# Kernel optimization log

Measured on AMD Instinct MI355X. Metric: run time of the kernel, lower is better.

## Reference

```python
import jax, jax.numpy as jnp
import numpy as np

NUM_HEADS = 16
NUM_BUCKETS = 32
MAX_DISTANCE = 128


def _rel_bucket(rel):
    # bidirectional T5-style relative position bucketing
    nb = NUM_BUCKETS // 2
    ret = (rel > 0).astype(jnp.int32) * nb
    n = jnp.abs(rel)
    max_exact = nb // 2
    is_small = n < max_exact
    safe = jnp.maximum(n, 1).astype(jnp.float32)
    large = max_exact + (jnp.log(safe / max_exact) / np.log(MAX_DISTANCE / max_exact) * (nb - max_exact)).astype(jnp.int32)
    large = jnp.minimum(large, nb - 1)
    return ret + jnp.where(is_small, n, large)


def setup_inputs() -> dict:
    key = jax.random.key(0)
    ks = jax.random.split(key, 12)
    S, B, E = 1024, 4, 1024
    D = E // NUM_HEADS
    s = 0.02
    return {
        "query": jax.random.normal(ks[0], (S, B, E), jnp.float32),
        "q_w": jax.random.normal(ks[1], (E, E), jnp.float32) * s,
        "q_b": jnp.zeros((E,), jnp.float32),
        "k_w": jax.random.normal(ks[2], (E, E), jnp.float32) * s,
        "k_b": jnp.zeros((E,), jnp.float32),
        "v_w": jax.random.normal(ks[3], (E, E), jnp.float32) * s,
        "v_b": jnp.zeros((E,), jnp.float32),
        "out_w": jax.random.normal(ks[4], (E, E), jnp.float32) * s,
        "out_b": jnp.zeros((E,), jnp.float32),
        "rel_emb": jax.random.normal(ks[5], (NUM_BUCKETS, NUM_HEADS), jnp.float32) * s,
        "grep_w": jax.random.normal(ks[6], (8, D), jnp.float32) * s,
        "grep_b": jnp.zeros((8,), jnp.float32),
        "grep_a": jnp.ones((NUM_HEADS,), jnp.float32),
    }


def reference(query, q_w, q_b, k_w, k_b, v_w, v_b, out_w, out_b, rel_emb, grep_w, grep_b, grep_a):
    S, B, E = query.shape
    H = NUM_HEADS
    D = E // H
    scaling = D ** -0.5

    q = (query @ q_w.T + q_b) * scaling  # scaling applied before gating, as in WavLM
    k = query @ k_w.T + k_b
    v = query @ v_w.T + v_b

    def split(x):  # (S,B,E) -> (B,H,S,D)
        return x.reshape(S, B, H, D).transpose(1, 2, 0, 3)

    q4, k4, v4 = split(q), split(k), split(v)

    attn = jnp.einsum('bhqd,bhkd->bhqk', q4, k4)  # (B,H,S,S)

    pos = jnp.arange(S)
    bucket = _rel_bucket(pos[None, :] - pos[:, None])  # (S,S)
    pbias = rel_emb[bucket].transpose(2, 0, 1)          # (H,S,S)

    # GRU-gated relative position scaling
    g = jnp.einsum('bhsd,ed->bhse', q4, grep_w) + grep_b      # (B,H,S,8)
    g = jax.nn.sigmoid(g.reshape(B, H, S, 2, 4).sum(-1))     # (B,H,S,2)
    gate_a, gate_b = g[..., 0], g[..., 1]
    gate = gate_a * (gate_b * grep_a[None, :, None] - 1.0) + 2.0  # (B,H,S)

    attn = attn + gate[..., None] * pbias[None]
    probs = jax.nn.softmax(attn, axis=-1)
    ctx = jnp.einsum('bhqk,bhkd->bhqd', probs, v4)  # (B,H,S,D)
    out = ctx.transpose(2, 0, 1, 3).reshape(S, B, E) @ out_w.T + out_b
    return out
```

## Files before the change

### kernel.cpp

```cpp
#include <hip/hip_runtime.h>
#include <hip/hip_bf16.h>
#include <stdint.h>


typedef short bf16x8 __attribute__((ext_vector_type(8)));
typedef _Float16 f16x8 __attribute__((ext_vector_type(8)));
typedef float f32x4 __attribute__((ext_vector_type(4)));
typedef float f32x16 __attribute__((ext_vector_type(16)));
typedef unsigned uint32x2 __attribute__((ext_vector_type(2)));

#define MFMA_BF16(a, b, c) __builtin_amdgcn_mfma_f32_16x16x32_bf16((a), (b), (c), 0, 0, 0)
#define MFMA_F16(a, b, c) __builtin_amdgcn_mfma_f32_16x16x32_f16((a), (b), (c), 0, 0, 0)
#define MFMA32_BF16(a, b, c) __builtin_amdgcn_mfma_f32_32x32x16_bf16((a), (b), (c), 0, 0, 0)

#define LOG2E 1.44269504088896f
#define LN2 0.693147180559945f

__device__ __forceinline__ unsigned short f2bf(float x) {
  union { float f; unsigned u; } v; v.f = x;
  unsigned r = v.u + 0x7fffu + ((v.u >> 16) & 1u);
  return (unsigned short)(r >> 16);
}
__device__ __forceinline__ float bf2f(unsigned short u) {
  union { unsigned u; float f; } v; v.u = ((unsigned)u) << 16;
  return v.f;
}
__device__ __forceinline__ unsigned short f2h(float x) {
  union { _Float16 h; unsigned short u; } v; v.h = (_Float16)x;
  return v.u;
}
__device__ __forceinline__ unsigned pk_bf2(float a, float b) {
  union { __hip_bfloat162 h2; unsigned u; } v;
  v.h2 = __float22bfloat162_rn(float2{a, b});
  return v.u;
}

__device__ __forceinline__ void gload_lds16(const void* g, void* l) {
  __builtin_amdgcn_global_load_lds(
      (const __attribute__((address_space(1))) unsigned int*)g,
      (__attribute__((address_space(3))) unsigned int*)l, 16, 0, 0);
}

__device__ __forceinline__ int swz(int row) { return (row ^ (row >> 2)) & 3; }

__global__ __launch_bounds__(256) void prep_kernel(
    const float* __restrict__ query, const float* __restrict__ q_w,
    const float* __restrict__ k_w, const float* __restrict__ v_w,
    const float* __restrict__ out_w, const float* __restrict__ rel_emb,
    unsigned short* __restrict__ q_bf, unsigned short* __restrict__ wq,
    unsigned short* __restrict__ wk, unsigned short* __restrict__ wv,
    unsigned short* __restrict__ ow_h,
    float* __restrict__ bias_f) {
  int i = blockIdx.x * 256 + threadIdx.x;
  if (i < 1048576) {
    int e4 = (i & 255) << 2;
    int sb = i >> 8;
    int s = sb >> 2, b = sb & 3;
    float4 q4 = *(const float4*)(query + ((size_t)i << 2));
    ushort4 o;
    o.x = f2bf(q4.x); o.y = f2bf(q4.y); o.z = f2bf(q4.z); o.w = f2bf(q4.w);
    *(ushort4*)&q_bf[((size_t)(b * 1024 + s) << 10) | e4] = o;
  } else if (i < 1310720) {
    int j = (i - 1048576) << 2;
    float4 a = *(const float4*)(q_w + j);
    float4 b = *(const float4*)(k_w + j);
    float4 c = *(const float4*)(v_w + j);
    float4 d = *(const float4*)(out_w + j);
    ushort4 o;
    o.x = f2bf(a.x); o.y = f2bf(a.y); o.z = f2bf(a.z); o.w = f2bf(a.w);
    *(ushort4*)&wq[j] = o;
    o.x = f2bf(b.x); o.y = f2bf(b.y); o.z = f2bf(b.z); o.w = f2bf(b.w);
    *(ushort4*)&wk[j] = o;
    o.x = f2bf(c.x); o.y = f2bf(c.y); o.z = f2bf(c.z); o.w = f2bf(c.w);
    *(ushort4*)&wv[j] = o;
    o.x = f2h(d.x); o.y = f2h(d.y); o.z = f2h(d.z); o.w = f2h(d.w);
    *(ushort4*)&ow_h[j] = o;
  } else {
    int idx = i - 1310720;
    if (idx >= 2056) return;
    if (idx >= 2047) {
#pragma unroll
      for (int h = 0; h < 16; ++h) bias_f[h * 2056 + idx] = 0.f;
      return;
    }
    int rel = idx - 1023;
    int n = rel < 0 ? -rel : rel;
    int ret = rel > 0 ? 16 : 0;
    int bucket;
    if (n < 8) {
      bucket = ret + n;
    } else {
      int large = 8 + (int)(logf((float)n / 8.0f) / logf(16.0f) * 8.0f);
      if (large > 15) large = 15;
      bucket = ret + large;
    }
#pragma unroll
    for (int h = 0; h < 16; ++h)
      bias_f[h * 2056 + idx] = rel_emb[bucket * 16 + h] * LOG2E;
  }
}

__global__ __launch_bounds__(256, 3) void qkv_gemm_kernel(
    const unsigned short* __restrict__ A, const unsigned short* __restrict__ Wq,
    const unsigned short* __restrict__ Wk, const unsigned short* __restrict__ Wv,
    const float* __restrict__ qb, const float* __restrict__ kb, const float* __restrict__ vb,
    unsigned short* __restrict__ qh,
    unsigned short* __restrict__ kh,
    unsigned short* __restrict__ vT)
{
  __shared__ __align__(16) char smem[32768];
  const int tid = threadIdx.x, lane = tid & 63;
  const int wv_ = tid >> 6;
  const int nt = blockIdx.x;
  const int mt = blockIdx.y;
  const int mat = nt >> 3;
  const unsigned short* W = mat == 0 ? Wq : (mat == 1 ? Wk : Wv);
  const int n0 = (nt & 7) * 128;
  const int m0 = mt * 128;
  const int moff = (wv_ & 1) * 64;
  const int noff = (wv_ >> 1) * 64;
  const int q15 = lane & 15, quad = lane >> 4;

  const int abase = (mat < 2) ? 8192 : 0;
  const int bbase2 = 8192 - abase;
  const int aoff = (mat < 2) ? noff : moff;
  const int boff = (mat < 2) ? moff : noff;

  f32x4 acc[4][4] = {};
  const char* Ab = (const char*)A;
  const char* Wb = (const char*)W;

  int st_row[2], st_g[2];
#pragma unroll
  for (int c = 0; c < 2; ++c) {
    int o = c * 4096 + tid * 16;
    int row = o >> 6, p = (o >> 4) & 3;
    st_row[c] = row;
    st_g[c] = p ^ swz(row);
  }

#define QKV_STAGE(kt, buf)                                                     \
  {                                                                            \
    char* bb = smem + (buf)*16384;                                             \
    _Pragma("unroll") for (int c = 0; c < 2; ++c) {                            \
      int o = c * 4096 + tid * 16;                                             \
      size_t ga = (size_t)(m0 + st_row[c]) * 2048 + (size_t)(kt)*64 + st_g[c] * 16; \
      size_t gb = (size_t)(n0 + st_row[c]) * 2048 + (size_t)(kt)*64 + st_g[c] * 16; \
      gload_lds16(Ab + ga, bb + o);                                            \
      gload_lds16(Wb + gb, bb + 8192 + o);                                     \
    }                                                                          \
  }

  QKV_STAGE(0, 0);
  for (int kt = 0; kt < 32; ++kt) {
    __syncthreads();
    const char* base = smem + (kt & 1) * 16384;
    if (kt < 31) QKV_STAGE(kt + 1, (kt + 1) & 1);

    bf16x8 af[4], bfr[4];
#pragma unroll
    for (int i = 0; i < 4; ++i) {
      int ra = aoff + i * 16 + q15;
      int rb = boff + i * 16 + q15;
      af[i] = *(const bf16x8*)(base + abase + ra * 64 + ((quad ^ swz(ra)) << 4));
      bfr[i] = *(const bf16x8*)(base + bbase2 + rb * 64 + ((quad ^ swz(rb)) << 4));
    }
#pragma unroll
    for (int i = 0; i < 4; ++i)
#pragma unroll
      for (int j = 0; j < 4; ++j) acc[i][j] = MFMA_BF16(af[i], bfr[j], acc[i][j]);
  }
#undef QKV_STAGE

  const int bidx = m0 >> 10;
  if (mat < 2) {
    const float* barr = mat == 0 ? qb : kb;
    unsigned short* dst = mat == 0 ? qh : kh;
    const float scale = mat == 0 ? (0.125f * LOG2E) : 1.0f;
    const int sA = (m0 & 1023) + moff + q15;
    const int nA = n0 + noff + (quad << 2);
#pragma unroll
    for (int i = 0; i < 4; ++i) {
      int colb = nA + i * 16;
      int hh = colb >> 6, dd = colb & 63;
      float bs0 = barr[colb + 0] * scale;
      float bs1 = barr[colb + 1] * scale;
      float bs2 = barr[colb + 2] * scale;
      float bs3 = barr[colb + 3] * scale;
#pragma unroll
      for (int j = 0; j < 4; ++j) {
        int s = sA + j * 16;
        ushort4 pk;
        pk.x = f2bf(__builtin_fmaf(acc[i][j][0], scale, bs0));
        pk.y = f2bf(__builtin_fmaf(acc[i][j][1], scale, bs1));
        pk.z = f2bf(__builtin_fmaf(acc[i][j][2], scale, bs2));
        pk.w = f2bf(__builtin_fmaf(acc[i][j][3], scale, bs3));
        *(ushort4*)&dst[((size_t)(bidx * 16 + hh) * 1024 + s) * 64 + dd] = pk;
      }
    }
  } else {
    const int s00 = (m0 & 1023) + moff + (quad << 2);
    const int c0 = n0 + noff + q15;
#pragma unroll
    for (int j = 0; j < 4; ++j) {
      int col = c0 + j * 16;
      int hh = col >> 6, dd = col & 63;
      float bias = vb[col];
#pragma unroll
      for (int i = 0; i < 4; ++i) {
        int s = s00 + i * 16;
        ushort4 pk;
        pk.x = f2bf(acc[i][j][0] + bias);
        pk.y = f2bf(acc[i][j][1] + bias);
        pk.z = f2bf(acc[i][j][2] + bias);
        pk.w = f2bf(acc[i][j][3] + bias);
        *(ushort4*)&vT[((size_t)(bidx * 16 + hh) * 64 + dd) * 1024 + s] = pk;
      }
    }
  }
}

__global__ __launch_bounds__(256) void gate_kernel(const unsigned short* __restrict__ qh,
                                                   const float* __restrict__ grep_w,
                                                   const float* __restrict__ grep_b,
                                                   const float* __restrict__ grep_a,
                                                   float* __restrict__ gate) {
  __shared__ float gw[512];
  __shared__ float gbb[8];
  __shared__ float gaa[16];
  int tid = threadIdx.x;
  for (int i = tid; i < 512; i += 256) gw[i] = grep_w[i];
  if (tid < 8) gbb[tid] = grep_b[tid];
  if (tid < 16) gaa[tid] = grep_a[tid];
  __syncthreads();
  int idx = blockIdx.x * 256 + tid;
  int h = (idx >> 10) & 15;
  const unsigned short* qrow = qh + (size_t)idx * 64;
  float a[8] = {0.f, 0.f, 0.f, 0.f, 0.f, 0.f, 0.f, 0.f};
#pragma unroll
  for (int c = 0; c < 8; ++c) {
    bf16x8 v = *(const bf16x8*)(qrow + c * 8);
#pragma unroll
    for (int jj = 0; jj < 8; ++jj) {
      float qv = bf2f((unsigned short)v[jj]);
      int d = c * 8 + jj;
#pragma unroll
      for (int e = 0; e < 8; ++e) a[e] += qv * gw[e * 64 + d];
    }
  }
  float sa = (a[0] + a[1] + a[2] + a[3]) * LN2 + gbb[0] + gbb[1] + gbb[2] + gbb[3];
  float sb = (a[4] + a[5] + a[6] + a[7]) * LN2 + gbb[4] + gbb[5] + gbb[6] + gbb[7];
  float siga = 1.f / (1.f + __expf(-sa));
  float sigb = 1.f / (1.f + __expf(-sb));
  gate[idx] = siga * (sigb * gaa[h] - 1.f) + 2.f;
}

__global__ __launch_bounds__(512, 4) void attn_kernel(
    const unsigned short* __restrict__ qh, const unsigned short* __restrict__ kh,
    const unsigned short* __restrict__ vT, const float* __restrict__ gate,
    const float* __restrict__ bias_f, unsigned short* __restrict__ ctx) {
  __shared__ __align__(16) char smem[37888];
  const int tid = threadIdx.x, lane = tid & 63, w = tid >> 6;
  const int qt = w >> 1, khalf = w & 1;
  const int bh = blockIdx.x;
  const int h = bh & 15;
  const int qs0 = blockIdx.y * 128;
  const int q31 = lane & 31, hb = lane >> 5, q7 = q31 & 7;
  const int sq = qs0 + qt * 32 + q31;

  float* bcf = (float*)(smem + 33280);
  {
    const float* gb = bias_f + h * 2056 + (896 - qs0);
    for (int i = tid; i < 1152; i += 512) bcf[i] = gb[i];
  }

  const char* kbase = (const char*)(kh + (size_t)bh * 65536);
  const char* vbase = (const char*)(vT + (size_t)bh * 65536);

  const int o = tid * 16;
  const int srow = o >> 7;
  const int sg = ((o >> 4) & 7) ^ (srow & 7);
  const size_t koff = (size_t)srow * 128 + sg * 16;
  const size_t voff = (size_t)srow * 2048 + sg * 16;

  gload_lds16(kbase + koff, smem + o);
  gload_lds16(vbase + voff, smem + 16384 + o);

  const unsigned short* qrow = qh + ((size_t)bh * 1024 + sq) * 64 + hb * 8;
  bf16x8 qf[4];
#pragma unroll
  for (int dc = 0; dc < 4; ++dc) qf[dc] = *(const bf16x8*)(qrow + dc * 16);

  const float gate_lane = gate[bh * 1024 + sq];

  const int i0 = (qs0 + 127 - sq) + khalf * 32 + hb * 4;

  float l_run = 0.f;
  f32x16 accO0 = {}, accO1 = {};

  for (int kc = 0; kc < 16; ++kc) {
    __syncthreads();
    const char* Kc = smem + (kc & 1) * 8192;
    const char* Vc = smem + 16384 + (kc & 1) * 8192;
    if (kc < 15) {
      int nb = (kc + 1) & 1;
      gload_lds16(kbase + (size_t)(kc + 1) * 8192 + koff, smem + nb * 8192 + o);
      gload_lds16(vbase + (size_t)(kc + 1) * 128 + voff, smem + 16384 + nb * 8192 + o);
    }

    f32x16 sac;
    {
      const int ib = i0 + kc * 64;
#pragma unroll
      for (int rg = 0; rg < 4; ++rg) {
        sac[rg * 4 + 0] = gate_lane * bcf[ib + rg * 8 + 0];
        sac[rg * 4 + 1] = gate_lane * bcf[ib + rg * 8 + 1];
        sac[rg * 4 + 2] = gate_lane * bcf[ib + rg * 8 + 2];
        sac[rg * 4 + 3] = gate_lane * bcf[ib + rg * 8 + 3];
      }
    }

    const char* Krow = Kc + (khalf * 32 + q31) * 128;
#pragma unroll
    for (int ks = 0; ks < 4; ++ks) {
      bf16x8 kf = *(const bf16x8*)(Krow + (((ks * 2 + hb) ^ q7) << 4));
      sac = MFMA32_BF16(kf, qf[ks], sac);
    }

    float ps = 0.f;
    unsigned pu[8];
#pragma unroll
    for (int rg = 0; rg < 4; ++rg) {
      float p0 = __builtin_exp2f(sac[rg * 4 + 0]);
      float p1 = __builtin_exp2f(sac[rg * 4 + 1]);
      float p2 = __builtin_exp2f(sac[rg * 4 + 2]);
      float p3 = __builtin_exp2f(sac[rg * 4 + 3]);
      ps += (p0 + p1) + (p2 + p3);
      pu[2 * rg] = pk_bf2(p0, p1);
      pu[2 * rg + 1] = pk_bf2(p2, p3);
    }
    l_run += ps;

    uint32x2 s02 = __builtin_amdgcn_permlane32_swap(pu[0], pu[2], false, false);
    uint32x2 s13 = __builtin_amdgcn_permlane32_swap(pu[1], pu[3], false, false);
    uint32x2 s46 = __builtin_amdgcn_permlane32_swap(pu[4], pu[6], false, false);
    uint32x2 s57 = __builtin_amdgcn_permlane32_swap(pu[5], pu[7], false, false);
    union PB { unsigned u[4]; bf16x8 v; } b0, b1;
    b0.u[0] = s02.x; b0.u[1] = s13.x; b0.u[2] = s02.y; b0.u[3] = s13.y;
    b1.u[0] = s46.x; b1.u[1] = s57.x; b1.u[2] = s46.y; b1.u[3] = s57.y;

#pragma unroll
    for (int mf = 0; mf < 2; ++mf) {
      bf16x8 pb = mf ? b1.v : b0.v;
      int vch = ((khalf * 4 + mf * 2 + hb) ^ q7) << 4;
      bf16x8 v0f = *(const bf16x8*)(Vc + q31 * 128 + vch);
      bf16x8 v1f = *(const bf16x8*)(Vc + (32 + q31) * 128 + vch);
      accO0 = MFMA32_BF16(v0f, pb, accO0);
      accO1 = MFMA32_BF16(v1f, pb, accO1);
    }
  }

  l_run += __shfl_xor(l_run, 32, 64);

  __syncthreads();
  float* Ot = (float*)smem;
  float* ow = Ot + (qt * 32 + q31) * 65;
  if (khalf == 0) {
#pragma unroll
    for (int rr = 0; rr < 16; ++rr) {
      int d = (rr & 3) + 8 * (rr >> 2) + 4 * hb;
      ow[d] = accO0[rr];
      ow[32 + d] = accO1[rr];
    }
    if (hb == 0) ow[64] = l_run;
  }
  __syncthreads();
  if (khalf == 1) {
    float inv = 1.0f / (ow[64] + l_run);
#pragma unroll
    for (int rr = 0; rr < 16; ++rr) {
      int d = (rr & 3) + 8 * (rr >> 2) + 4 * hb;
      ow[d] = (ow[d] + accO0[rr]) * inv;
      ow[32 + d] = (ow[32 + d] + accO1[rr]) * inv;
    }
  }
  __syncthreads();
  {
    int row = tid >> 2, dg = tid & 3;
    int s = qs0 + row;
    const float* src = Ot + row * 65 + dg * 16;
    unsigned short hbuf[16];
#pragma unroll
    for (int j = 0; j < 16; ++j) hbuf[j] = f2h(src[j]);
    size_t base = (size_t)(s * 4 + (bh >> 4)) * 1024 + h * 64 + dg * 16;
    *(uint4*)(ctx + base) = *(const uint4*)(hbuf);
    *(uint4*)(ctx + base + 8) = *(const uint4*)(hbuf + 8);
  }
}

__global__ __launch_bounds__(256, 3) void outproj_kernel(
    const unsigned short* __restrict__ Af,
    const unsigned short* __restrict__ Bf,
    const float* __restrict__ ob, float* __restrict__ out) {
  __shared__ __align__(16) char smem[24576];
  const int tid = threadIdx.x, lane = tid & 63, wv_ = tid >> 6;
  const int q15 = lane & 15, quad = lane >> 4;
  const int n0 = blockIdx.x * 128;
  const int m0 = blockIdx.y * 64;
  const int moff = (wv_ & 1) * 32;
  const int noff = (wv_ >> 1) * 64;

  const int oa = tid * 16;
  const int ra_ = oa >> 6;
  const int ga_ = (((oa >> 4) & 3) ^ swz(ra_)) << 4;
  int rb_[2], gb_[2], obo_[2];
#pragma unroll
  for (int c = 0; c < 2; ++c) {
    int ob2 = c * 4096 + tid * 16;
    obo_[c] = ob2;
    rb_[c] = ob2 >> 6;
    gb_[c] = (((ob2 >> 4) & 3) ^ swz(rb_[c])) << 4;
  }

#define OP_STAGE(kt, buf)                                                        \
  {                                                                              \
    char* bb = smem + (buf)*12288;                                               \
    size_t ga = (size_t)(m0 + ra_) * 2048 + (size_t)(kt)*64 + ga_;               \
    gload_lds16((const char*)Af + ga, bb + oa);                                  \
    _Pragma("unroll") for (int c = 0; c < 2; ++c) {                              \
      size_t gb = (size_t)(n0 + rb_[c]) * 2048 + (size_t)(kt)*64 + gb_[c];       \
      gload_lds16((const char*)Bf + gb, bb + 4096 + obo_[c]);                    \
    }                                                                            \
  }

  f32x4 acc[4][2] = {};
  OP_STAGE(0, 0);
  for (int kt = 0; kt < 32; ++kt) {
    __syncthreads();
    const char* base = smem + (kt & 1) * 12288;
    if (kt < 31) OP_STAGE(kt + 1, (kt + 1) & 1);

    f16x8 wf[4], cf[2];
#pragma unroll
    for (int i = 0; i < 4; ++i) {
      int rb = noff + i * 16 + q15;
      wf[i] = *(const f16x8*)(base + 4096 + rb * 64 + ((quad ^ swz(rb)) << 4));
    }
#pragma unroll
    for (int j = 0; j < 2; ++j) {
      int ra = moff + j * 16 + q15;
      cf[j] = *(const f16x8*)(base + ra * 64 + ((quad ^ swz(ra)) << 4));
    }
#pragma unroll
    for (int i = 0; i < 4; ++i)
#pragma unroll
      for (int j = 0; j < 2; ++j) acc[i][j] = MFMA_F16(wf[i], cf[j], acc[i][j]);
  }
#undef OP_STAGE

  const int sA = m0 + moff + q15;
  const int nA = n0 + noff + (quad << 2);
#pragma unroll
  for (int i = 0; i < 4; ++i) {
    int colb = nA + i * 16;
    float4 b4 = *(const float4*)&ob[colb];
#pragma unroll
    for (int j = 0; j < 2; ++j) {
      int s = sA + j * 16;
      float4 o4;
      o4.x = acc[i][j][0] + b4.x;
      o4.y = acc[i][j][1] + b4.y;
      o4.z = acc[i][j][2] + b4.z;
      o4.w = acc[i][j][3] + b4.w;
      *(float4*)&out[(size_t)s * 1024 + colb] = o4;
    }
  }
}

extern "C" void kernel_launch(void* const* d_in, const int* in_sizes, int n_in,
                              void* d_out, int out_size, void* d_ws, size_t ws_size,
                              hipStream_t stream) {
  const float* query = (const float*)d_in[0];
  const float* q_w = (const float*)d_in[1];
  const float* q_b = (const float*)d_in[2];
  const float* k_w = (const float*)d_in[3];
  const float* k_b = (const float*)d_in[4];
  const float* v_w = (const float*)d_in[5];
  const float* v_b = (const float*)d_in[6];
  const float* out_w = (const float*)d_in[7];
  const float* out_b = (const float*)d_in[8];
  const float* rel_emb = (const float*)d_in[9];
  const float* grep_w = (const float*)d_in[10];
  const float* grep_b = (const float*)d_in[11];
  const float* grep_a = (const float*)d_in[12];
  float* out = (float*)d_out;

  const size_t MB = 1u << 20;
  char* ws = (char*)d_ws;
  unsigned short* q_bf = (unsigned short*)(ws);
  unsigned short* wq_bf = (unsigned short*)(ws + 8 * MB);
  unsigned short* wk_bf = (unsigned short*)(ws + 10 * MB);
  unsigned short* wv_bf = (unsigned short*)(ws + 12 * MB);
  unsigned short* ow_h = (unsigned short*)(ws + 14 * MB);
  unsigned short* qhp = (unsigned short*)(ws + 16 * MB);
  unsigned short* khp = (unsigned short*)(ws + 24 * MB);
  unsigned short* vTp = (unsigned short*)(ws + 32 * MB);
  unsigned short* ctxp = (unsigned short*)(ws + 40 * MB);
  float* gatep = (float*)(ws + 48 * MB);
  float* biasp = (float*)(ws + 48 * MB + 256 * 1024);

  prep_kernel<<<5129, 256, 0, stream>>>(query, q_w, k_w, v_w, out_w, rel_emb, q_bf, wq_bf,
                                        wk_bf, wv_bf, ow_h, biasp);
  qkv_gemm_kernel<<<dim3(24, 32), 256, 0, stream>>>(q_bf, wq_bf, wk_bf, wv_bf, q_b, k_b, v_b,
                                                    qhp, khp, vTp);
  gate_kernel<<<256, 256, 0, stream>>>(qhp, grep_w, grep_b, grep_a, gatep);
  attn_kernel<<<dim3(64, 8), 512, 0, stream>>>(qhp, khp, vTp, gatep, biasp, ctxp);
  outproj_kernel<<<dim3(8, 64), 256, 0, stream>>>(ctxp, ow_h, out_b, out);
}
```

Baseline: 193.0 us.

## Triple-buffer K/V tiles in attention kernel with explicit vmcnt waits and MFMA priority

Replaces the double-buffered K/V LDS staging with a three-stage ring: two chunks are prefetched up front and each iteration issues the load two chunks ahead, waiting only on the older loads with s_waitcnt vmcnt before a raw barrier. It also raises wave priority around the MFMA blocks. The aim is to hide global-to-LDS load latency better and keep the matrix units busy. The cost is larger LDS use (53760 bytes per block), which may lower occupancy below the launch-bounds target of 4 blocks.

```diff
diff --git a/kernel.cpp b/kernel.cpp
--- a/kernel.cpp
+++ b/kernel.cpp
@@ -259,7 +259,7 @@
     const unsigned short* __restrict__ qh, const unsigned short* __restrict__ kh,
     const unsigned short* __restrict__ vT, const float* __restrict__ gate,
     const float* __restrict__ bias_f, unsigned short* __restrict__ ctx) {
-  __shared__ __align__(16) char smem[37888];
+  __shared__ __align__(16) char smem[53760];
   const int tid = threadIdx.x, lane = tid & 63, w = tid >> 6;
   const int qt = w >> 1, khalf = w & 1;
   const int bh = blockIdx.x;
@@ -268,7 +268,7 @@
   const int q31 = lane & 31, hb = lane >> 5, q7 = q31 & 7;
   const int sq = qs0 + qt * 32 + q31;
 
-  float* bcf = (float*)(smem + 33280);
+  float* bcf = (float*)(smem + 49152);
   {
     const float* gb = bias_f + h * 2056 + (896 - qs0);
     for (int i = tid; i < 1152; i += 512) bcf[i] = gb[i];
@@ -283,8 +283,11 @@
   const size_t koff = (size_t)srow * 128 + sg * 16;
   const size_t voff = (size_t)srow * 2048 + sg * 16;
 
-  gload_lds16(kbase + koff, smem + o);
-  gload_lds16(vbase + voff, smem + 16384 + o);
+#define ATT_STAGE(kcn, buf)                                                        \
+  {                                                                                \
+    gload_lds16(kbase + (size_t)(kcn)*8192 + koff, smem + (buf)*8192 + o);         \
+    gload_lds16(vbase + (size_t)(kcn)*128 + voff, smem + 24576 + (buf)*8192 + o);  \
+  }
 
   const unsigned short* qrow = qh + ((size_t)bh * 1024 + sq) * 64 + hb * 8;
   bf16x8 qf[4];
@@ -298,15 +301,22 @@
   float l_run = 0.f;
   f32x16 accO0 = {}, accO1 = {};
 
+  __syncthreads();
+  ATT_STAGE(0, 0);
+  ATT_STAGE(1, 1);
+
+  int cb = 0, sb = 2;
   for (int kc = 0; kc < 16; ++kc) {
-    __syncthreads();
-    const char* Kc = smem + (kc & 1) * 8192;
-    const char* Vc = smem + 16384 + (kc & 1) * 8192;
     if (kc < 15) {
-      int nb = (kc + 1) & 1;
-      gload_lds16(kbase + (size_t)(kc + 1) * 8192 + koff, smem + nb * 8192 + o);
-      gload_lds16(vbase + (size_t)(kc + 1) * 128 + voff, smem + 16384 + nb * 8192 + o);
-    }
+      asm volatile("s_waitcnt vmcnt(2)" ::: "memory");
+    } else {
+      asm volatile("s_waitcnt vmcnt(0)" ::: "memory");
+    }
+    __builtin_amdgcn_s_barrier();
+    __builtin_amdgcn_sched_barrier(0);
+    const char* Kc = smem + cb * 8192;
+    const char* Vc = smem + 24576 + cb * 8192;
+    if (kc < 14) ATT_STAGE(kc + 2, sb);
 
     f32x16 sac;
     {
@@ -321,11 +331,13 @@
     }
 
     const char* Krow = Kc + (khalf * 32 + q31) * 128;
+    __builtin_amdgcn_s_setprio(1);
 #pragma unroll
     for (int ks = 0; ks < 4; ++ks) {
       bf16x8 kf = *(const bf16x8*)(Krow + (((ks * 2 + hb) ^ q7) << 4));
       sac = MFMA32_BF16(kf, qf[ks], sac);
     }
+    __builtin_amdgcn_s_setprio(0);
 
     float ps = 0.f;
     unsigned pu[8];
@@ -349,6 +361,7 @@
     b0.u[0] = s02.x; b0.u[1] = s13.x; b0.u[2] = s02.y; b0.u[3] = s13.y;
     b1.u[0] = s46.x; b1.u[1] = s57.x; b1.u[2] = s46.y; b1.u[3] = s57.y;
 
+    __builtin_amdgcn_s_setprio(1);
 #pragma unroll
     for (int mf = 0; mf < 2; ++mf) {
       bf16x8 pb = mf ? b1.v : b0.v;
@@ -358,7 +371,12 @@
       accO0 = MFMA32_BF16(v0f, pb, accO0);
       accO1 = MFMA32_BF16(v1f, pb, accO1);
     }
-  }
+    __builtin_amdgcn_s_setprio(0);
+
+    cb = cb == 2 ? 0 : cb + 1;
+    sb = sb == 2 ? 0 : sb + 1;
+  }
+#undef ATT_STAGE
 
   l_run += __shfl_xor(l_run, 32, 64);
 
```

Result: no change. 195.5 us (+1.3%).

## Load K/V fragments directly from global memory, dropping LDS staging and barriers

Applied to the files above, without the earlier changes.

The attention loop no longer stages K and V tiles through double-buffered LDS with async global-to-LDS copies and a barrier every iteration. Each lane now reads its MFMA operand fragments straight from global memory, with no per-iteration synchronisation. The MFMA groups are wrapped in s_setprio to raise wave priority during matrix work. The cost is redundant global or L2 reads, since the two k-half waves per q-tile fetch overlapping V data, and load latency is no longer hidden by explicit prefetch.

```diff
diff --git a/kernel.cpp b/kernel.cpp
--- a/kernel.cpp
+++ b/kernel.cpp
@@ -265,7 +265,7 @@
   const int bh = blockIdx.x;
   const int h = bh & 15;
   const int qs0 = blockIdx.y * 128;
-  const int q31 = lane & 31, hb = lane >> 5, q7 = q31 & 7;
+  const int q31 = lane & 31, hb = lane >> 5;
   const int sq = qs0 + qt * 32 + q31;
 
   float* bcf = (float*)(smem + 33280);
@@ -274,17 +274,10 @@
     for (int i = tid; i < 1152; i += 512) bcf[i] = gb[i];
   }
 
-  const char* kbase = (const char*)(kh + (size_t)bh * 65536);
-  const char* vbase = (const char*)(vT + (size_t)bh * 65536);
-
-  const int o = tid * 16;
-  const int srow = o >> 7;
-  const int sg = ((o >> 4) & 7) ^ (srow & 7);
-  const size_t koff = (size_t)srow * 128 + sg * 16;
-  const size_t voff = (size_t)srow * 2048 + sg * 16;
-
-  gload_lds16(kbase + koff, smem + o);
-  gload_lds16(vbase + voff, smem + 16384 + o);
+  const char* kb0 = (const char*)(kh + (size_t)bh * 65536) +
+                    (khalf * 32 + q31) * 128 + hb * 16;
+  const char* vb0 = (const char*)(vT + (size_t)bh * 65536) +
+                    q31 * 2048 + (khalf * 4 + hb) * 16;
 
   const unsigned short* qrow = qh + ((size_t)bh * 1024 + sq) * 64 + hb * 8;
   bf16x8 qf[4];
@@ -298,15 +291,19 @@
   float l_run = 0.f;
   f32x16 accO0 = {}, accO1 = {};
 
+  __syncthreads();
+
   for (int kc = 0; kc < 16; ++kc) {
-    __syncthreads();
-    const char* Kc = smem + (kc & 1) * 8192;
-    const char* Vc = smem + 16384 + (kc & 1) * 8192;
-    if (kc < 15) {
-      int nb = (kc + 1) & 1;
-      gload_lds16(kbase + (size_t)(kc + 1) * 8192 + koff, smem + nb * 8192 + o);
-      gload_lds16(vbase + (size_t)(kc + 1) * 128 + voff, smem + 16384 + nb * 8192 + o);
-    }
+    const char* kp = kb0 + kc * 8192;
+    bf16x8 kf0 = *(const bf16x8*)(kp);
+    bf16x8 kf1 = *(const bf16x8*)(kp + 32);
+    bf16x8 kf2 = *(const bf16x8*)(kp + 64);
+    bf16x8 kf3 = *(const bf16x8*)(kp + 96);
+    const char* vp = vb0 + kc * 128;
+    bf16x8 v00 = *(const bf16x8*)(vp);
+    bf16x8 v10 = *(const bf16x8*)(vp + 65536);
+    bf16x8 v01 = *(const bf16x8*)(vp + 32);
+    bf16x8 v11 = *(const bf16x8*)(vp + 65536 + 32);
 
     f32x16 sac;
     {
@@ -320,12 +317,12 @@
       }
     }
 
-    const char* Krow = Kc + (khalf * 32 + q31) * 128;
-#pragma unroll
-    for (int ks = 0; ks < 4; ++ks) {
-      bf16x8 kf = *(const bf16x8*)(Krow + (((ks * 2 + hb) ^ q7) << 4));
-      sac = MFMA32_BF16(kf, qf[ks], sac);
-    }
+    __builtin_amdgcn_s_setprio(1);
+    sac = MFMA32_BF16(kf0, qf[0], sac);
+    sac = MFMA32_BF16(kf1, qf[1], sac);
+    sac = MFMA32_BF16(kf2, qf[2], sac);
+    sac = MFMA32_BF16(kf3, qf[3], sac);
+    __builtin_amdgcn_s_setprio(0);
 
     float ps = 0.f;
     unsigned pu[8];
@@ -349,15 +346,12 @@
     b0.u[0] = s02.x; b0.u[1] = s13.x; b0.u[2] = s02.y; b0.u[3] = s13.y;
     b1.u[0] = s46.x; b1.u[1] = s57.x; b1.u[2] = s46.y; b1.u[3] = s57.y;
 
-#pragma unroll
-    for (int mf = 0; mf < 2; ++mf) {
-      bf16x8 pb = mf ? b1.v : b0.v;
-      int vch = ((khalf * 4 + mf * 2 + hb) ^ q7) << 4;
-      bf16x8 v0f = *(const bf16x8*)(Vc + q31 * 128 + vch);
-      bf16x8 v1f = *(const bf16x8*)(Vc + (32 + q31) * 128 + vch);
-      accO0 = MFMA32_BF16(v0f, pb, accO0);
-      accO1 = MFMA32_BF16(v1f, pb, accO1);
-    }
+    __builtin_amdgcn_s_setprio(1);
+    accO0 = MFMA32_BF16(v00, b0.v, accO0);
+    accO1 = MFMA32_BF16(v10, b0.v, accO1);
+    accO0 = MFMA32_BF16(v01, b1.v, accO0);
+    accO1 = MFMA32_BF16(v11, b1.v, accO1);
+    __builtin_amdgcn_s_setprio(0);
   }
 
   l_run += __shfl_xor(l_run, 32, 64);
```

Measured after the change: 230.8 us. +19.6%, slower.
